# Kernel tuning notes

Measured on AMD Instinct MI355X. Metric: run time of the kernel, lower is better.

The kernel has to match this reference:

```python
import jax, jax.numpy as jnp
import numpy as np

N, E, H, G, L = 100000, 200000, 32, 100, 4
NODE_IN, EDGE_IN, NGRAPH = 6, 4, 50
EPS = 1e-5

def setup_inputs() -> dict:
    key = jax.random.key(0)
    ks = jax.random.split(key, 32)
    s = 0.05
    inp = {
        "x": jax.random.normal(ks[0], (N, NODE_IN), jnp.float32),
        "edge_index": jax.random.randint(ks[1], (2, E), 0, N, jnp.int64),
        "edge_attr": jax.random.normal(ks[2], (E, EDGE_IN), jnp.float32),
        "batch": jnp.sort(jax.random.randint(ks[3], (N,), 0, NGRAPH, jnp.int64)),
        # node embedding: Linear + ReLU + BatchNorm1d
        "w_embed": jax.random.normal(ks[4], (NODE_IN, H), jnp.float32) * s,
        "b_embed": jnp.zeros((H,), jnp.float32),
        "bn_gamma": jnp.ones((H,), jnp.float32),
        "bn_beta": jnp.zeros((H,), jnp.float32),
        # NNConv layers (stacked over L): edge MLP Linear(EDGE_IN,2H)->ReLU->Linear(2H,H*H), root weight, bias
        "conv_w1": jax.random.normal(ks[5], (L, EDGE_IN, 2 * H), jnp.float32) * s,
        "conv_b1": jnp.zeros((L, 2 * H), jnp.float32),
        "conv_w2": jax.random.normal(ks[6], (L, 2 * H, H * H), jnp.float32) * s,
        "conv_b2": jnp.zeros((L, H * H), jnp.float32),
        "conv_root": jax.random.normal(ks[7], (L, H, H), jnp.float32) * s,
        "conv_bias": jnp.zeros((L, H), jnp.float32),
        # heads
        "wk_w1": jax.random.normal(ks[8], (H, H), jnp.float32) * s,
        "wk_b1": jnp.zeros((H,), jnp.float32),
        "wk_w2": jax.random.normal(ks[9], (H, 1), jnp.float32) * s,
        "wk_b2": jnp.zeros((1,), jnp.float32),
        "uj_w1": jax.random.normal(ks[10], (H, H), jnp.float32) * s,
        "uj_b1": jnp.zeros((H,), jnp.float32),
        "uj_w2": jax.random.normal(ks[11], (H, G), jnp.float32) * s,
        "uj_b2": jnp.zeros((G,), jnp.float32),
        "zk_w1": jax.random.normal(ks[12], (H, H), jnp.float32) * s,
        "zk_b1": jnp.zeros((H,), jnp.float32),
        "zk_w2": jax.random.normal(ks[13], (H, G), jnp.float32) * s,
        "zk_b2": jnp.zeros((G,), jnp.float32),
    }
    return inp

def _mlp2(h, w1, b1, w2, b2):
    return jax.nn.relu(h @ w1 + b1) @ w2 + b2

def _forward(x, edge_index, edge_attr, batch,
             w_embed, b_embed, bn_gamma, bn_beta,
             conv_w1, conv_b1, conv_w2, conv_b2, conv_root, conv_bias,
             wk_w1, wk_b1, wk_w2, wk_b2,
             uj_w1, uj_b1, uj_w2, uj_b2,
             zk_w1, zk_b1, zk_w2, zk_b2):
    src, dst = edge_index[0], edge_index[1]
    # node embed: Linear -> ReLU -> BatchNorm1d (training-mode batch stats)
    h = jax.nn.relu(x @ w_embed + b_embed)
    mu = h.mean(axis=0)
    var = ((h - mu) ** 2).mean(axis=0)  # biased, as torch BN uses for normalization
    h = (h - mu) * jax.lax.rsqrt(var + EPS) * bn_gamma + bn_beta
    # in-degree for mean aggregation
    deg = jax.ops.segment_sum(jnp.ones((E,), h.dtype), dst, num_segments=N)
    inv_deg = (1.0 / jnp.maximum(deg, 1.0))[:, None]
    for l in range(L):
        # per-edge weight matrix from edge MLP: [E, H, H]
        W = _mlp2(edge_attr, conv_w1[l], conv_b1[l], conv_w2[l], conv_b2[l]).reshape(E, H, H)
        msg = jnp.einsum('ei,eio->eo', h[src], W)  # gather + per-edge matmul
        agg = jax.ops.segment_sum(msg, dst, num_segments=N) * inv_deg  # scatter-mean
        h = jax.nn.relu(agg + h @ conv_root[l] + conv_bias[l])
    # global mean pool over graphs
    cnt = jax.ops.segment_sum(jnp.ones((N,), h.dtype), batch, num_segments=NGRAPH)
    hg = jax.ops.segment_sum(h, batch, num_segments=NGRAPH) / jnp.maximum(cnt, 1.0)[:, None]
    wk = _mlp2(hg, wk_w1, wk_b1, wk_w2, wk_b2).squeeze(-1)
    uj = _mlp2(hg, uj_w1, uj_b1, uj_w2, uj_b2)
    zk = _mlp2(hg, zk_w1, zk_b1, zk_w2, zk_b2)
    return wk, uj, zk

def reference(x, edge_index, edge_attr, batch,
              w_embed, b_embed, bn_gamma, bn_beta,
              conv_w1, conv_b1, conv_w2, conv_b2, conv_root, conv_bias,
              wk_w1, wk_b1, wk_w2, wk_b2,
              uj_w1, uj_b1, uj_w2, uj_b2,
              zk_w1, zk_b1, zk_w2, zk_b2):
    return _forward(x, edge_index, edge_attr, batch,
                    w_embed, b_embed, bn_gamma, bn_beta,
                    conv_w1, conv_b1, conv_w2, conv_b2, conv_root, conv_bias,
                    wk_w1, wk_b1, wk_w2, wk_b2,
                    uj_w1, uj_b1, uj_w2, uj_b2,
                    zk_w1, zk_b1, zk_w2, zk_b2)
```

## Files before the change

### kernel.cpp

```cpp
#include <hip/hip_runtime.h>

#define NN 100000
#define NE 200000
#define HH 32
#define NL 4
#define NGR 50
#define GOUT 100
#define NODE_IN 6
#define NEB 782

typedef __attribute__((ext_vector_type(8))) short bf16x8;
typedef __attribute__((ext_vector_type(4))) float f32x4;

__device__ __forceinline__ unsigned short bf16_rne(float x) {
    unsigned int b = __float_as_uint(x);
    b += 0x7FFFu + ((b >> 16) & 1u);
    return (unsigned short)(b >> 16);
}
__device__ __forceinline__ float bf16_f(unsigned short h) {
    return __uint_as_float(((unsigned int)h) << 16);
}

__global__ __launch_bounds__(256) void split_w2(const float* __restrict__ w2,
                                                unsigned short* __restrict__ w2h,
                                                unsigned short* __restrict__ w2l)
{
    int id = blockIdx.x * 256 + threadIdx.x;
    if (id >= NL * 64 * 1024) return;
    int l = id >> 16, rem = id & 65535;
    int k = rem >> 10, n = rem & 1023;
    float v = w2[id];
    unsigned short hi = bf16_rne(v);
    float lov = v - bf16_f(hi);
    unsigned short lo = bf16_rne(lov);
    int out = l * 65536 + n * 64 + k;
    w2h[out] = hi;
    w2l[out] = lo;
}

__global__ __launch_bounds__(256) void embed_kernel(
    const float* __restrict__ x, const float* __restrict__ w,
    const float* __restrict__ b, float* __restrict__ h0)
{
    int nid = blockIdx.x * 256 + threadIdx.x;
    if (nid >= NN) return;
    float xv[NODE_IN];
    #pragma unroll
    for (int d = 0; d < NODE_IN; ++d) xv[d] = x[nid * NODE_IN + d];
    float4* op = (float4*)(h0 + (size_t)nid * HH);
    #pragma unroll
    for (int q = 0; q < 8; ++q) {
        float4 r;
        float* rp = (float*)&r;
        #pragma unroll
        for (int u = 0; u < 4; ++u) {
            int j = q * 4 + u;
            float a = b[j];
            #pragma unroll
            for (int d = 0; d < NODE_IN; ++d) a = fmaf(xv[d], w[d * HH + j], a);
            rp[u] = fmaxf(a, 0.f);
        }
        op[q] = r;
    }
}

__global__ __launch_bounds__(256) void stats_kernel(const float* __restrict__ h0,
                                                    float* __restrict__ stats)
{
    __shared__ float ls[64];
    int tid = threadIdx.x;
    if (tid < 64) ls[tid] = 0.f;
    __syncthreads();
    float s[4] = {0.f, 0.f, 0.f, 0.f};
    float q[4] = {0.f, 0.f, 0.f, 0.f};
    const float4* h4 = (const float4*)h0;
    const int total = NN * HH / 4;
    for (int idx = blockIdx.x * 256 + tid; idx < total; idx += 128 * 256) {
        float4 v = h4[idx];
        s[0] += v.x; q[0] += v.x * v.x;
        s[1] += v.y; q[1] += v.y * v.y;
        s[2] += v.z; q[2] += v.z * v.z;
        s[3] += v.w; q[3] += v.w * v.w;
    }
    int c0 = (tid * 4) & 31;
    #pragma unroll
    for (int u = 0; u < 4; ++u) {
        atomicAdd(&ls[c0 + u], s[u]);
        atomicAdd(&ls[32 + c0 + u], q[u]);
    }
    __syncthreads();
    if (tid < 64) unsafeAtomicAdd(&stats[tid], ls[tid]);
}

__global__ __launch_bounds__(256) void degi_kernel(const int* __restrict__ ei,
                                                   int* __restrict__ degi)
{
    int e = blockIdx.x * 256 + threadIdx.x;
    if (e >= NE) return;
    atomicAdd(&degi[ei[NE + e]], 1);
}

__global__ void bn_finalize(const float* __restrict__ stats,
                            const float* __restrict__ gamma,
                            const float* __restrict__ beta,
                            float* __restrict__ bnp)
{
    int j = threadIdx.x;
    if (j >= HH) return;
    const float invn = 1.0f / (float)NN;
    float mu  = stats[j] * invn;
    float var = stats[32 + j] * invn - mu * mu;
    float rs  = 1.0f / sqrtf(var + 1e-5f);
    float sc  = rs * gamma[j];
    bnp[j]      = sc;
    bnp[32 + j] = beta[j] - mu * sc;
}

__global__ __launch_bounds__(256) void bn_apply(float* __restrict__ h,
                                                const float* __restrict__ bnp)
{
    int idx = blockIdx.x * 256 + threadIdx.x;
    if (idx >= NN * HH / 4) return;
    float4 v = ((float4*)h)[idx];
    int j = (idx * 4) & 31;
    v.x = fmaf(v.x, bnp[j + 0], bnp[32 + j + 0]);
    v.y = fmaf(v.y, bnp[j + 1], bnp[32 + j + 1]);
    v.z = fmaf(v.z, bnp[j + 2], bnp[32 + j + 2]);
    v.w = fmaf(v.w, bnp[j + 3], bnp[32 + j + 3]);
    ((float4*)h)[idx] = v;
}

__global__ __launch_bounds__(256) void scan1(const int* __restrict__ degi,
                                             int* __restrict__ rowptr,
                                             int* __restrict__ bsum)
{
    __shared__ int sd[256];
    int tid = threadIdx.x;
    int i = blockIdx.x * 256 + tid;
    int v = (i < NN) ? degi[i] : 0;
    sd[tid] = v;
    __syncthreads();
    #pragma unroll
    for (int off = 1; off < 256; off <<= 1) {
        int t = (tid >= off) ? sd[tid - off] : 0;
        __syncthreads();
        sd[tid] += t;
        __syncthreads();
    }
    if (i < NN) rowptr[i] = sd[tid] - v;
    if (tid == 255) bsum[blockIdx.x] = sd[255];
}

__global__ __launch_bounds__(512) void scan2(int* __restrict__ bsum)
{
    __shared__ int sd[512];
    int tid = threadIdx.x;
    int v = (tid < 391) ? bsum[tid] : 0;
    sd[tid] = v;
    __syncthreads();
    #pragma unroll
    for (int off = 1; off < 512; off <<= 1) {
        int t = (tid >= off) ? sd[tid - off] : 0;
        __syncthreads();
        sd[tid] += t;
        __syncthreads();
    }
    if (tid < 391) bsum[tid] = sd[tid] - v;
}

__global__ __launch_bounds__(256) void scan3(int* __restrict__ rowptr,
                                             const int* __restrict__ bsum,
                                             int* __restrict__ cursor)
{
    int i = blockIdx.x * 256 + threadIdx.x;
    if (i < NN) {
        int r = rowptr[i] + bsum[blockIdx.x];
        rowptr[i] = r;
        cursor[i] = r;
    }
    if (i == 0) rowptr[NN] = NE;
}

__global__ __launch_bounds__(256) void scatter_k(const int* __restrict__ ei,
                                                 int* __restrict__ cursor,
                                                 int* __restrict__ perm)
{
    int e = blockIdx.x * 256 + threadIdx.x;
    if (e >= NE) return;
    int d = ei[NE + e];
    int pos = atomicAdd(&cursor[d], 1);
    perm[pos] = e;
}

__global__ __launch_bounds__(512, 3) void edge_mfma(
    const float* __restrict__ h, const int* __restrict__ ei,
    const float* __restrict__ ea, const int* __restrict__ perm,
    const float* __restrict__ w1, const float* __restrict__ b1,
    const unsigned short* __restrict__ w2h, const unsigned short* __restrict__ w2l,
    const float* __restrict__ b2, float* __restrict__ msg)
{
    __shared__ float hT[32 * 256];
    __shared__ float b2l[1024];
    __shared__ unsigned short Bh[4096];
    __shared__ unsigned short Bl[4096];

    const int tid  = threadIdx.x;
    const int w    = tid >> 6;
    const int lane = tid & 63;
    const int l15  = lane & 15;
    const int lg   = lane >> 4;
    const int eb   = blockIdx.x * 256;
    const int wb32 = w * 32;

    const unsigned int* gh = (const unsigned int*)w2h;
    const unsigned int* gl = (const unsigned int*)w2l;

    auto stage = [&](int c2) {
        int g = tid;
        int n = g >> 3, j = g & 7;
        int gi = ((c2 * 64 + n) << 3) + (j ^ (n & 7));
        int lb = (tid & ~63) * 8;
        __builtin_amdgcn_global_load_lds(
            (const __attribute__((address_space(1))) unsigned int*)(gh + (size_t)gi * 4),
            (__attribute__((address_space(3))) unsigned int*)(&Bh[0] + lb), 16, 0, 0);
        __builtin_amdgcn_global_load_lds(
            (const __attribute__((address_space(1))) unsigned int*)(gl + (size_t)gi * 4),
            (__attribute__((address_space(3))) unsigned int*)(&Bl[0] + lb), 16, 0, 0);
    };

    {
        int eloc = tid & 255;
        int half = tid >> 8;
        int e = eb + eloc;
        int pe = (e < NE) ? perm[e] : 0;
        int s  = (e < NE) ? ei[pe] : 0;
        const float4* hp = (const float4*)(h + (size_t)s * HH) + half * 4;
        #pragma unroll
        for (int q = 0; q < 4; ++q) {
            float4 v = hp[q];
            int col = half * 16 + q * 4;
            hT[(col + 0) * 256 + eloc] = v.x;
            hT[(col + 1) * 256 + eloc] = v.y;
            hT[(col + 2) * 256 + eloc] = v.z;
            hT[(col + 3) * 256 + eloc] = v.w;
        }
        if (tid < 256) ((float4*)b2l)[tid] = ((const float4*)b2)[tid];
    }

    bf16x8 thi[2][2], tlo[2][2];
    #pragma unroll
    for (int et = 0; et < 2; ++et) {
        int e2 = eb + wb32 + et * 16 + l15;
        bool ev = (e2 < NE);
        int pe2 = ev ? perm[e2] : 0;
        float4 eav = make_float4(0.f, 0.f, 0.f, 0.f);
        if (ev) eav = *(const float4*)(ea + (size_t)pe2 * 4);
        #pragma unroll
        for (int ks = 0; ks < 2; ++ks) {
            int k0 = ks * 32 + lg * 8;
            #pragma unroll
            for (int j = 0; j < 8; ++j) {
                float t = b1[k0 + j];
                t = fmaf(eav.x, w1[0 * 64 + k0 + j], t);
                t = fmaf(eav.y, w1[1 * 64 + k0 + j], t);
                t = fmaf(eav.z, w1[2 * 64 + k0 + j], t);
                t = fmaf(eav.w, w1[3 * 64 + k0 + j], t);
                t = ev ? fmaxf(t, 0.f) : 0.f;
                unsigned short hi = bf16_rne(t);
                float lov = t - bf16_f(hi);
                unsigned short lo = bf16_rne(lov);
                thi[et][ks][j] = (short)hi;
                tlo[et][ks][j] = (short)lo;
            }
        }
    }

    float acc0[2][4], acc1[2][4];
    #pragma unroll
    for (int et = 0; et < 2; ++et)
        #pragma unroll
        for (int r = 0; r < 4; ++r) { acc0[et][r] = 0.f; acc1[et][r] = 0.f; }

    for (int c2 = 0; c2 < 16; ++c2) {
        __syncthreads();
        stage(c2);
        __syncthreads();

        #pragma unroll
        for (int ntp = 0; ntp < 2; ++ntp) {
            const int i = c2 * 2 + ntp;
            float4 h4[2];
            #pragma unroll
            for (int et = 0; et < 2; ++et)
                h4[et] = *(const float4*)&hT[i * 256 + wb32 + et * 16 + lg * 4];
            #pragma unroll
            for (int half = 0; half < 2; ++half) {
                int nt = ntp * 2 + half;
                int nl = nt * 16 + l15;
                int swz = (nl & 7) << 4;
                const char* bhrow = (const char*)&Bh[0] + nl * 128;
                const char* blrow = (const char*)&Bl[0] + nl * 128;
                bf16x8 Bh0 = *(const bf16x8*)(bhrow + (( 0 + lg * 16) ^ swz));
                bf16x8 Bl0 = *(const bf16x8*)(blrow + (( 0 + lg * 16) ^ swz));
                bf16x8 Bh1 = *(const bf16x8*)(bhrow + ((64 + lg * 16) ^ swz));
                bf16x8 Bl1 = *(const bf16x8*)(blrow + ((64 + lg * 16) ^ swz));
                float b2v = b2l[c2 * 64 + nt * 16 + l15];
                #pragma unroll
                for (int et = 0; et < 2; ++et) {
                    f32x4 G = {0.f, 0.f, 0.f, 0.f};
                    G = __builtin_amdgcn_mfma_f32_16x16x32_bf16(thi[et][0], Bh0, G, 0, 0, 0);
                    G = __builtin_amdgcn_mfma_f32_16x16x32_bf16(tlo[et][0], Bh0, G, 0, 0, 0);
                    G = __builtin_amdgcn_mfma_f32_16x16x32_bf16(thi[et][0], Bl0, G, 0, 0, 0);
                    G = __builtin_amdgcn_mfma_f32_16x16x32_bf16(thi[et][1], Bh1, G, 0, 0, 0);
                    G = __builtin_amdgcn_mfma_f32_16x16x32_bf16(tlo[et][1], Bh1, G, 0, 0, 0);
                    G = __builtin_amdgcn_mfma_f32_16x16x32_bf16(thi[et][1], Bl1, G, 0, 0, 0);
                    if (half == 0) {
                        acc0[et][0] = fmaf(h4[et].x, G[0] + b2v, acc0[et][0]);
                        acc0[et][1] = fmaf(h4[et].y, G[1] + b2v, acc0[et][1]);
                        acc0[et][2] = fmaf(h4[et].z, G[2] + b2v, acc0[et][2]);
                        acc0[et][3] = fmaf(h4[et].w, G[3] + b2v, acc0[et][3]);
                    } else {
                        acc1[et][0] = fmaf(h4[et].x, G[0] + b2v, acc1[et][0]);
                        acc1[et][1] = fmaf(h4[et].y, G[1] + b2v, acc1[et][1]);
                        acc1[et][2] = fmaf(h4[et].z, G[2] + b2v, acc1[et][2]);
                        acc1[et][3] = fmaf(h4[et].w, G[3] + b2v, acc1[et][3]);
                    }
                }
            }
        }
    }

    #pragma unroll
    for (int et = 0; et < 2; ++et) {
        #pragma unroll
        for (int r = 0; r < 4; ++r) {
            int row = eb + wb32 + et * 16 + lg * 4 + r;
            if (row < NE) {
                msg[(size_t)row * HH + l15]      = acc0[et][r];
                msg[(size_t)row * HH + 16 + l15] = acc1[et][r];
            }
        }
    }
}

__global__ __launch_bounds__(256) void node_kernel(
    const float* __restrict__ h, const float* __restrict__ msg,
    const int* __restrict__ rowptr, const float* __restrict__ root,
    const float* __restrict__ bias, float* __restrict__ hout)
{
    int nid = blockIdx.x * 256 + threadIdx.x;
    if (nid >= NN) return;
    int j0 = rowptr[nid], j1 = rowptr[nid + 1];
    float hv[HH];
    {
        const float4* hp = (const float4*)(h + (size_t)nid * HH);
        #pragma unroll
        for (int q = 0; q < 8; ++q) {
            float4 v = hp[q];
            hv[4*q+0] = v.x; hv[4*q+1] = v.y; hv[4*q+2] = v.z; hv[4*q+3] = v.w;
        }
    }
    float acc[HH];
    #pragma unroll
    for (int o = 0; o < HH; ++o) acc[o] = bias[o];
    #pragma unroll
    for (int i = 0; i < HH; ++i) {
        float hi = hv[i];
        #pragma unroll
        for (int o = 0; o < HH; ++o) acc[o] = fmaf(hi, root[i * HH + o], acc[o]);
    }
    float s[HH];
    #pragma unroll
    for (int o = 0; o < HH; ++o) s[o] = 0.f;
    for (int j = j0; j < j1; ++j) {
        const float4* mp = (const float4*)(msg + (size_t)j * HH);
        #pragma unroll
        for (int q = 0; q < 8; ++q) {
            float4 m = mp[q];
            s[4*q+0] += m.x; s[4*q+1] += m.y; s[4*q+2] += m.z; s[4*q+3] += m.w;
        }
    }
    float inv = 1.0f / fmaxf((float)(j1 - j0), 1.0f);
    float4* op = (float4*)(hout + (size_t)nid * HH);
    #pragma unroll
    for (int q = 0; q < 8; ++q) {
        float4 r;
        r.x = fmaxf(fmaf(s[4*q+0], inv, acc[4*q+0]), 0.f);
        r.y = fmaxf(fmaf(s[4*q+1], inv, acc[4*q+1]), 0.f);
        r.z = fmaxf(fmaf(s[4*q+2], inv, acc[4*q+2]), 0.f);
        r.w = fmaxf(fmaf(s[4*q+3], inv, acc[4*q+3]), 0.f);
        op[q] = r;
    }
}

__global__ __launch_bounds__(256) void pool_kernel(
    const float* __restrict__ h, const int* __restrict__ batch,
    float* __restrict__ pool, float* __restrict__ cnt)
{
    __shared__ float lp[NGR * HH];
    __shared__ float lc[NGR];
    int tid = threadIdx.x;
    for (int i = tid; i < NGR * HH; i += 256) lp[i] = 0.f;
    if (tid < NGR) lc[tid] = 0.f;
    __syncthreads();
    int c = tid & 31, grp = tid >> 5;
    int base = blockIdx.x * 1024 + grp * 128;
    int curg = -1;
    float acc = 0.f, cn = 0.f;
    for (int s = 0; s < 128; ++s) {
        int n = base + s;
        if (n >= NN) break;
        int g = batch[n];
        if (g != curg) {
            if (curg >= 0) {
                atomicAdd(&lp[curg * HH + c], acc);
                if (c == 0) atomicAdd(&lc[curg], cn);
            }
            curg = g; acc = 0.f; cn = 0.f;
        }
        acc += h[(size_t)n * HH + c];
        cn += 1.f;
    }
    if (curg >= 0) {
        atomicAdd(&lp[curg * HH + c], acc);
        if (c == 0) atomicAdd(&lc[curg], cn);
    }
    __syncthreads();
    for (int i = tid; i < NGR * HH; i += 256)
        if (lp[i] != 0.f) unsafeAtomicAdd(&pool[i], lp[i]);
    if (tid < NGR && lc[tid] != 0.f) unsafeAtomicAdd(&cnt[tid], lc[tid]);
}

__global__ __launch_bounds__(256) void heads_kernel(
    const float* __restrict__ pool, const float* __restrict__ cnt,
    const float* __restrict__ wkw1, const float* __restrict__ wkb1,
    const float* __restrict__ wkw2, const float* __restrict__ wkb2,
    const float* __restrict__ ujw1, const float* __restrict__ ujb1,
    const float* __restrict__ ujw2, const float* __restrict__ ujb2,
    const float* __restrict__ zkw1, const float* __restrict__ zkb1,
    const float* __restrict__ zkw2, const float* __restrict__ zkb2,
    float* __restrict__ out)
{
    __shared__ float hg[NGR * HH];
    __shared__ float hid[NGR * HH];
    int tid = threadIdx.x;
    int head = blockIdx.x;
    const float *w1, *b1, *w2, *b2;
    if (head == 0)      { w1 = wkw1; b1 = wkb1; w2 = wkw2; b2 = wkb2; }
    else if (head == 1) { w1 = ujw1; b1 = ujb1; w2 = ujw2; b2 = ujb2; }
    else                { w1 = zkw1; b1 = zkb1; w2 = zkw2; b2 = zkb2; }
    for (int i = tid; i < NGR * HH; i += 256) {
        int g = i >> 5;
        hg[i] = pool[i] / fmaxf(cnt[g], 1.0f);
    }
    __syncthreads();
    for (int i = tid; i < NGR * HH; i += 256) {
        int g = i >> 5, c = i & 31;
        float a = b1[c];
        for (int j = 0; j < HH; ++j) a = fmaf(hg[g * HH + j], w1[j * HH + c], a);
        hid[i] = fmaxf(a, 0.f);
    }
    __syncthreads();
    if (head == 0) {
        if (tid < NGR) {
            float a = b2[0];
            for (int c = 0; c < HH; ++c) a = fmaf(hid[tid * HH + c], w2[c], a);
            out[tid] = a;
        }
    } else {
        float* ob = out + NGR + (head - 1) * NGR * GOUT;
        for (int i = tid; i < NGR * GOUT; i += 256) {
            int g = i / GOUT, u = i % GOUT;
            float a = b2[u];
            for (int c = 0; c < HH; ++c) a = fmaf(hid[g * HH + c], w2[c * GOUT + u], a);
            ob[i] = a;
        }
    }
}

extern "C" void kernel_launch(void* const* d_in, const int* in_sizes, int n_in,
                              void* d_out, int out_size, void* d_ws, size_t ws_size,
                              hipStream_t stream)
{
    const float* x     = (const float*)d_in[0];
    const int*   ei    = (const int*)d_in[1];
    const float* ea    = (const float*)d_in[2];
    const int*   batch = (const int*)d_in[3];
    const float* w_emb = (const float*)d_in[4];
    const float* b_emb = (const float*)d_in[5];
    const float* gamma = (const float*)d_in[6];
    const float* beta  = (const float*)d_in[7];
    const float* cw1   = (const float*)d_in[8];
    const float* cb1   = (const float*)d_in[9];
    const float* cw2   = (const float*)d_in[10];
    const float* cb2   = (const float*)d_in[11];
    const float* croot = (const float*)d_in[12];
    const float* cbias = (const float*)d_in[13];
    float* out = (float*)d_out;

    unsigned short* w2h = (unsigned short*)d_ws;
    unsigned short* w2l = w2h + 262144;
    float* msg    = (float*)(w2l + 262144);
    float* h0     = msg + (size_t)NE * HH;
    float* h1     = h0 + (size_t)NN * HH;
    int*   rowptr = (int*)(h1 + (size_t)NN * HH);
    int*   cursor = rowptr + 100004;
    int*   perm   = cursor + NN;
    int*   degi   = perm + NE;
    int*   bsum   = degi + NN;
    float* stats  = (float*)(bsum + 512);
    float* pool   = stats + 64;
    float* cnt    = pool + NGR * HH;
    float* bnp    = cnt + NGR;

    hipMemsetAsync(degi, 0, (size_t)(NN + 512 + 64 + NGR * HH + NGR) * sizeof(int), stream);

    split_w2<<<(NL * 65536) / 256, 256, 0, stream>>>(cw2, w2h, w2l);
    embed_kernel<<<(NN + 255) / 256, 256, 0, stream>>>(x, w_emb, b_emb, h0);
    stats_kernel<<<128, 256, 0, stream>>>(h0, stats);
    degi_kernel<<<NEB, 256, 0, stream>>>(ei, degi);
    bn_finalize<<<1, 32, 0, stream>>>(stats, gamma, beta, bnp);
    bn_apply<<<(NN * HH / 4 + 255) / 256, 256, 0, stream>>>(h0, bnp);

    scan1<<<391, 256, 0, stream>>>(degi, rowptr, bsum);
    scan2<<<1, 512, 0, stream>>>(bsum);
    scan3<<<391, 256, 0, stream>>>(rowptr, bsum, cursor);
    scatter_k<<<NEB, 256, 0, stream>>>(ei, cursor, perm);

    float* hc = h0;
    float* hn = h1;
    for (int l = 0; l < NL; ++l) {
        edge_mfma<<<NEB, 512, 0, stream>>>(
            hc, ei, ea, perm,
            cw1 + (size_t)l * 4 * 64, cb1 + (size_t)l * 64,
            w2h + (size_t)l * 65536, w2l + (size_t)l * 65536,
            cb2 + (size_t)l * 1024, msg);
        node_kernel<<<(NN + 255) / 256, 256, 0, stream>>>(
            hc, msg, rowptr, croot + (size_t)l * HH * HH, cbias + (size_t)l * HH, hn);
        float* t = hc; hc = hn; hn = t;
    }

    pool_kernel<<<(NN + 1023) / 1024, 256, 0, stream>>>(hc, batch, pool, cnt);
    heads_kernel<<<3, 256, 0, stream>>>(pool, cnt,
        (const float*)d_in[14], (const float*)d_in[15], (const float*)d_in[16], (const float*)d_in[17],
        (const float*)d_in[18], (const float*)d_in[19], (const float*)d_in[20], (const float*)d_in[21],
        (const float*)d_in[22], (const float*)d_in[23], (const float*)d_in[24], (const float*)d_in[25],
        out);
}
```

Baseline: 620.2 us.

## Precompute per-node bias term h·b2 and drop LDS transpose of source features

The edge-MLP bias contribution h_src·reshape(b2) depends only on the source node, so it is precomputed per node: in a fused BN-apply kernel for layer 0 and at the end of node_kernel for later layers. The edge kernel seeds its accumulators from that per-node value. The edge kernel also no longer stages transposed source features and b2 in LDS. Instead it reads two source features per chunk directly from global memory, swaps the MFMA operand order so each lane's output maps to contiguous edge-row columns, and writes msg with vector stores. This lowers LDS use and per-edge bias work, but adds extra global traffic and a 32x32 matvec per node in node_kernel, and drops the occupancy hint on the launch bounds.

```diff
diff --git a/kernel.cpp b/kernel.cpp
--- a/kernel.cpp
+++ b/kernel.cpp
@@ -116,18 +116,39 @@
     bnp[32 + j] = beta[j] - mu * sc;
 }
 
-__global__ __launch_bounds__(256) void bn_apply(float* __restrict__ h,
-                                                const float* __restrict__ bnp)
-{
-    int idx = blockIdx.x * 256 + threadIdx.x;
-    if (idx >= NN * HH / 4) return;
-    float4 v = ((float4*)h)[idx];
-    int j = (idx * 4) & 31;
-    v.x = fmaf(v.x, bnp[j + 0], bnp[32 + j + 0]);
-    v.y = fmaf(v.y, bnp[j + 1], bnp[32 + j + 1]);
-    v.z = fmaf(v.z, bnp[j + 2], bnp[32 + j + 2]);
-    v.w = fmaf(v.w, bnp[j + 3], bnp[32 + j + 3]);
-    ((float4*)h)[idx] = v;
+__global__ __launch_bounds__(256) void bn_b2h_kernel(
+    float* __restrict__ h, const float* __restrict__ bnp,
+    const float* __restrict__ b2, float* __restrict__ b2h)
+{
+    int nid = blockIdx.x * 256 + threadIdx.x;
+    if (nid >= NN) return;
+    float hv[HH];
+    float4* hp = (float4*)(h + (size_t)nid * HH);
+    #pragma unroll
+    for (int q = 0; q < 8; ++q) {
+        float4 v = hp[q];
+        int j = q * 4;
+        v.x = fmaf(v.x, bnp[j + 0], bnp[32 + j + 0]);
+        v.y = fmaf(v.y, bnp[j + 1], bnp[32 + j + 1]);
+        v.z = fmaf(v.z, bnp[j + 2], bnp[32 + j + 2]);
+        v.w = fmaf(v.w, bnp[j + 3], bnp[32 + j + 3]);
+        hp[q] = v;
+        hv[j+0] = v.x; hv[j+1] = v.y; hv[j+2] = v.z; hv[j+3] = v.w;
+    }
+    float4* bp = (float4*)(b2h + (size_t)nid * HH);
+    #pragma unroll
+    for (int q = 0; q < 8; ++q) {
+        float4 a = make_float4(0.f, 0.f, 0.f, 0.f);
+        #pragma unroll
+        for (int i = 0; i < HH; ++i) {
+            const float* br = b2 + i * HH + q * 4;
+            a.x = fmaf(hv[i], br[0], a.x);
+            a.y = fmaf(hv[i], br[1], a.y);
+            a.z = fmaf(hv[i], br[2], a.z);
+            a.w = fmaf(hv[i], br[3], a.w);
+        }
+        bp[q] = a;
+    }
 }
 
 __global__ __launch_bounds__(256) void scan1(const int* __restrict__ degi,
@@ -192,15 +213,13 @@
     perm[pos] = e;
 }
 
-__global__ __launch_bounds__(512, 3) void edge_mfma(
+__global__ __launch_bounds__(512) void edge_mfma(
     const float* __restrict__ h, const int* __restrict__ ei,
     const float* __restrict__ ea, const int* __restrict__ perm,
     const float* __restrict__ w1, const float* __restrict__ b1,
     const unsigned short* __restrict__ w2h, const unsigned short* __restrict__ w2l,
-    const float* __restrict__ b2, float* __restrict__ msg)
-{
-    __shared__ float hT[32 * 256];
-    __shared__ float b2l[1024];
+    const float* __restrict__ b2h, float* __restrict__ msg)
+{
     __shared__ unsigned short Bh[4096];
     __shared__ unsigned short Bl[4096];
 
@@ -228,31 +247,14 @@
             (__attribute__((address_space(3))) unsigned int*)(&Bl[0] + lb), 16, 0, 0);
     };
 
-    {
-        int eloc = tid & 255;
-        int half = tid >> 8;
-        int e = eb + eloc;
-        int pe = (e < NE) ? perm[e] : 0;
-        int s  = (e < NE) ? ei[pe] : 0;
-        const float4* hp = (const float4*)(h + (size_t)s * HH) + half * 4;
-        #pragma unroll
-        for (int q = 0; q < 4; ++q) {
-            float4 v = hp[q];
-            int col = half * 16 + q * 4;
-            hT[(col + 0) * 256 + eloc] = v.x;
-            hT[(col + 1) * 256 + eloc] = v.y;
-            hT[(col + 2) * 256 + eloc] = v.z;
-            hT[(col + 3) * 256 + eloc] = v.w;
-        }
-        if (tid < 256) ((float4*)b2l)[tid] = ((const float4*)b2)[tid];
-    }
-
+    int srcv[2];
     bf16x8 thi[2][2], tlo[2][2];
     #pragma unroll
     for (int et = 0; et < 2; ++et) {
         int e2 = eb + wb32 + et * 16 + l15;
         bool ev = (e2 < NE);
         int pe2 = ev ? perm[e2] : 0;
+        srcv[et] = ev ? ei[pe2] : 0;
         float4 eav = make_float4(0.f, 0.f, 0.f, 0.f);
         if (ev) eav = *(const float4*)(ea + (size_t)pe2 * 4);
         #pragma unroll
@@ -275,56 +277,53 @@
         }
     }
 
-    float acc0[2][4], acc1[2][4];
+    f32x4 acc[2][2];
     #pragma unroll
     for (int et = 0; et < 2; ++et)
         #pragma unroll
-        for (int r = 0; r < 4; ++r) { acc0[et][r] = 0.f; acc1[et][r] = 0.f; }
+        for (int p = 0; p < 2; ++p)
+            acc[et][p] = *(const f32x4*)(b2h + (size_t)srcv[et] * HH + p * 16 + lg * 4);
 
     for (int c2 = 0; c2 < 16; ++c2) {
+        float2 h2[2];
+        #pragma unroll
+        for (int et = 0; et < 2; ++et)
+            h2[et] = *(const float2*)(h + (size_t)srcv[et] * HH + 2 * c2);
+
         __syncthreads();
         stage(c2);
         __syncthreads();
 
         #pragma unroll
-        for (int ntp = 0; ntp < 2; ++ntp) {
-            const int i = c2 * 2 + ntp;
-            float4 h4[2];
+        for (int nt = 0; nt < 4; ++nt) {
+            int nl = nt * 16 + l15;
+            int swz = (nl & 7) << 4;
+            const char* bhrow = (const char*)&Bh[0] + nl * 128;
+            const char* blrow = (const char*)&Bl[0] + nl * 128;
+            bf16x8 Ah0 = *(const bf16x8*)(bhrow + (( 0 + lg * 16) ^ swz));
+            bf16x8 Al0 = *(const bf16x8*)(blrow + (( 0 + lg * 16) ^ swz));
+            bf16x8 Ah1 = *(const bf16x8*)(bhrow + ((64 + lg * 16) ^ swz));
+            bf16x8 Al1 = *(const bf16x8*)(blrow + ((64 + lg * 16) ^ swz));
             #pragma unroll
-            for (int et = 0; et < 2; ++et)
-                h4[et] = *(const float4*)&hT[i * 256 + wb32 + et * 16 + lg * 4];
-            #pragma unroll
-            for (int half = 0; half < 2; ++half) {
-                int nt = ntp * 2 + half;
-                int nl = nt * 16 + l15;
-                int swz = (nl & 7) << 4;
-                const char* bhrow = (const char*)&Bh[0] + nl * 128;
-                const char* blrow = (const char*)&Bl[0] + nl * 128;
-                bf16x8 Bh0 = *(const bf16x8*)(bhrow + (( 0 + lg * 16) ^ swz));
-                bf16x8 Bl0 = *(const bf16x8*)(blrow + (( 0 + lg * 16) ^ swz));
-                bf16x8 Bh1 = *(const bf16x8*)(bhrow + ((64 + lg * 16) ^ swz));
-                bf16x8 Bl1 = *(const bf16x8*)(blrow + ((64 + lg * 16) ^ swz));
-                float b2v = b2l[c2 * 64 + nt * 16 + l15];
-                #pragma unroll
-                for (int et = 0; et < 2; ++et) {
-                    f32x4 G = {0.f, 0.f, 0.f, 0.f};
-                    G = __builtin_amdgcn_mfma_f32_16x16x32_bf16(thi[et][0], Bh0, G, 0, 0, 0);
-                    G = __builtin_amdgcn_mfma_f32_16x16x32_bf16(tlo[et][0], Bh0, G, 0, 0, 0);
-                    G = __builtin_amdgcn_mfma_f32_16x16x32_bf16(thi[et][0], Bl0, G, 0, 0, 0);
-                    G = __builtin_amdgcn_mfma_f32_16x16x32_bf16(thi[et][1], Bh1, G, 0, 0, 0);
-                    G = __builtin_amdgcn_mfma_f32_16x16x32_bf16(tlo[et][1], Bh1, G, 0, 0, 0);
-                    G = __builtin_amdgcn_mfma_f32_16x16x32_bf16(thi[et][1], Bl1, G, 0, 0, 0);
-                    if (half == 0) {
-                        acc0[et][0] = fmaf(h4[et].x, G[0] + b2v, acc0[et][0]);
-                        acc0[et][1] = fmaf(h4[et].y, G[1] + b2v, acc0[et][1]);
-                        acc0[et][2] = fmaf(h4[et].z, G[2] + b2v, acc0[et][2]);
-                        acc0[et][3] = fmaf(h4[et].w, G[3] + b2v, acc0[et][3]);
-                    } else {
-                        acc1[et][0] = fmaf(h4[et].x, G[0] + b2v, acc1[et][0]);
-                        acc1[et][1] = fmaf(h4[et].y, G[1] + b2v, acc1[et][1]);
-                        acc1[et][2] = fmaf(h4[et].z, G[2] + b2v, acc1[et][2]);
-                        acc1[et][3] = fmaf(h4[et].w, G[3] + b2v, acc1[et][3]);
-                    }
+            for (int et = 0; et < 2; ++et) {
+                f32x4 G = {0.f, 0.f, 0.f, 0.f};
+                G = __builtin_amdgcn_mfma_f32_16x16x32_bf16(Ah0, thi[et][0], G, 0, 0, 0);
+                G = __builtin_amdgcn_mfma_f32_16x16x32_bf16(Ah0, tlo[et][0], G, 0, 0, 0);
+                G = __builtin_amdgcn_mfma_f32_16x16x32_bf16(Al0, thi[et][0], G, 0, 0, 0);
+                G = __builtin_amdgcn_mfma_f32_16x16x32_bf16(Ah1, thi[et][1], G, 0, 0, 0);
+                G = __builtin_amdgcn_mfma_f32_16x16x32_bf16(Ah1, tlo[et][1], G, 0, 0, 0);
+                G = __builtin_amdgcn_mfma_f32_16x16x32_bf16(Al1, thi[et][1], G, 0, 0, 0);
+                float hm = (nt < 2) ? h2[et].x : h2[et].y;
+                if ((nt & 1) == 0) {
+                    acc[et][0][0] = fmaf(hm, G[0], acc[et][0][0]);
+                    acc[et][0][1] = fmaf(hm, G[1], acc[et][0][1]);
+                    acc[et][0][2] = fmaf(hm, G[2], acc[et][0][2]);
+                    acc[et][0][3] = fmaf(hm, G[3], acc[et][0][3]);
+                } else {
+                    acc[et][1][0] = fmaf(hm, G[0], acc[et][1][0]);
+                    acc[et][1][1] = fmaf(hm, G[1], acc[et][1][1]);
+                    acc[et][1][2] = fmaf(hm, G[2], acc[et][1][2]);
+                    acc[et][1][3] = fmaf(hm, G[3], acc[et][1][3]);
                 }
             }
         }
@@ -332,13 +331,11 @@
 
     #pragma unroll
     for (int et = 0; et < 2; ++et) {
-        #pragma unroll
-        for (int r = 0; r < 4; ++r) {
-            int row = eb + wb32 + et * 16 + lg * 4 + r;
-            if (row < NE) {
-                msg[(size_t)row * HH + l15]      = acc0[et][r];
-                msg[(size_t)row * HH + 16 + l15] = acc1[et][r];
-            }
+        int e2 = eb + wb32 + et * 16 + l15;
+        if (e2 < NE) {
+            float* mrow = msg + (size_t)e2 * HH;
+            *(f32x4*)(mrow + lg * 4)      = acc[et][0];
+            *(f32x4*)(mrow + 16 + lg * 4) = acc[et][1];
         }
     }
 }
@@ -346,7 +343,8 @@
 __global__ __launch_bounds__(256) void node_kernel(
     const float* __restrict__ h, const float* __restrict__ msg,
     const int* __restrict__ rowptr, const float* __restrict__ root,
-    const float* __restrict__ bias, float* __restrict__ hout)
+    const float* __restrict__ bias, float* __restrict__ hout,
+    const float* __restrict__ b2n, float* __restrict__ b2hout, int do_b2h)
 {
     int nid = blockIdx.x * 256 + threadIdx.x;
     if (nid >= NN) return;
@@ -381,6 +379,7 @@
         }
     }
     float inv = 1.0f / fmaxf((float)(j1 - j0), 1.0f);
+    float ho[HH];
     float4* op = (float4*)(hout + (size_t)nid * HH);
     #pragma unroll
     for (int q = 0; q < 8; ++q) {
@@ -390,6 +389,23 @@
         r.z = fmaxf(fmaf(s[4*q+2], inv, acc[4*q+2]), 0.f);
         r.w = fmaxf(fmaf(s[4*q+3], inv, acc[4*q+3]), 0.f);
         op[q] = r;
+        ho[4*q+0] = r.x; ho[4*q+1] = r.y; ho[4*q+2] = r.z; ho[4*q+3] = r.w;
+    }
+    if (do_b2h) {
+        float4* bp = (float4*)(b2hout + (size_t)nid * HH);
+        #pragma unroll
+        for (int q = 0; q < 8; ++q) {
+            float4 a = make_float4(0.f, 0.f, 0.f, 0.f);
+            #pragma unroll
+            for (int i = 0; i < HH; ++i) {
+                const float* br = b2n + i * HH + q * 4;
+                a.x = fmaf(ho[i], br[0], a.x);
+                a.y = fmaf(ho[i], br[1], a.y);
+                a.z = fmaf(ho[i], br[2], a.z);
+                a.w = fmaf(ho[i], br[3], a.w);
+            }
+            bp[q] = a;
+        }
     }
 }
 
@@ -503,7 +519,8 @@
     float* msg    = (float*)(w2l + 262144);
     float* h0     = msg + (size_t)NE * HH;
     float* h1     = h0 + (size_t)NN * HH;
-    int*   rowptr = (int*)(h1 + (size_t)NN * HH);
+    float* b2h    = h1 + (size_t)NN * HH;
+    int*   rowptr = (int*)(b2h + (size_t)NN * HH);
     int*   cursor = rowptr + 100004;
     int*   perm   = cursor + NN;
     int*   degi   = perm + NE;
@@ -520,7 +537,7 @@
     stats_kernel<<<128, 256, 0, stream>>>(h0, stats);
     degi_kernel<<<NEB, 256, 0, stream>>>(ei, degi);
     bn_finalize<<<1, 32, 0, stream>>>(stats, gamma, beta, bnp);
-    bn_apply<<<(NN * HH / 4 + 255) / 256, 256, 0, stream>>>(h0, bnp);
+    bn_b2h_kernel<<<(NN + 255) / 256, 256, 0, stream>>>(h0, bnp, cb2, b2h);
 
     scan1<<<391, 256, 0, stream>>>(degi, rowptr, bsum);
     scan2<<<1, 512, 0, stream>>>(bsum);
@@ -534,9 +551,11 @@
             hc, ei, ea, perm,
             cw1 + (size_t)l * 4 * 64, cb1 + (size_t)l * 64,
             w2h + (size_t)l * 65536, w2l + (size_t)l * 65536,
-            cb2 + (size_t)l * 1024, msg);
+            b2h, msg);
+        int do_b2h = (l < NL - 1);
         node_kernel<<<(NN + 255) / 256, 256, 0, stream>>>(
-            hc, msg, rowptr, croot + (size_t)l * HH * HH, cbias + (size_t)l * HH, hn);
+            hc, msg, rowptr, croot + (size_t)l * HH * HH, cbias + (size_t)l * HH, hn,
+            cb2 + (size_t)(l + 1 < NL ? l + 1 : l) * 1024, b2h, do_b2h);
         float* t = hc; hc = hn; hn = t;
     }
 
```

Measured after the change: 1.448 ms. 133% more time.
